# Kernel tuning notes

Measured on AMD Instinct MI355X. Metric: run time of the kernel, lower is better.

Reference implementation:

```python
import jax, jax.numpy as jnp
import numpy as np

NUM_POPS = 8
K_ACTIVE = 2
IN, OUT = 2048, 2048
BATCH = 8192


def setup_inputs() -> dict:
    key = jax.random.key(0)
    ks = jax.random.split(key, 5)
    scale_in = 1.0 / np.sqrt(IN)
    return {
        "x": jax.random.normal(ks[0], (BATCH, IN), dtype=jnp.float32),
        # expert (population) linear params, stacked: W[p] is [OUT, IN]
        "W": jax.random.uniform(ks[1], (NUM_POPS, OUT, IN), dtype=jnp.float32, minval=-scale_in, maxval=scale_in),
        "b": jax.random.uniform(ks[2], (NUM_POPS, OUT), dtype=jnp.float32, minval=-scale_in, maxval=scale_in),
        # selector linear params
        "Ws": jax.random.uniform(ks[3], (NUM_POPS, IN), dtype=jnp.float32, minval=-scale_in, maxval=scale_in),
        "bs": jax.random.uniform(ks[4], (NUM_POPS,), dtype=jnp.float32, minval=-scale_in, maxval=scale_in),
    }


def reference(x, W, b, Ws, bs):
    # Eval-path math of SimplifiedDRNLayer: per-sample top-k expert selection,
    # uniform mean over the k selected experts' linear outputs.
    logits = x @ Ws.T + bs                      # [B, P]
    probs = jax.nn.softmax(logits, axis=-1)     # [B, P]
    _, topk_idx = jax.lax.top_k(probs, K_ACTIVE)  # [B, k] int32
    # combine weights: 1/k on selected experts, 0 elsewhere
    mask = jax.nn.one_hot(topk_idx, NUM_POPS, dtype=x.dtype).sum(axis=1) / K_ACTIVE  # [B, P]
    # all-expert outputs (P is small/fixed); [B, P, OUT]
    ys = jnp.einsum("poi,bi->bpo", W, x) + b
    out = jnp.einsum("bp,bpo->bo", mask, ys)    # [B, OUT]
    return out
```

## Files before the change

### kernel.cpp

```cpp
#include <hip/hip_runtime.h>
#include <stdint.h>

#define B_ROWS 8192
#define K_DIM 2048
#define N_DIM 2048
#define NPOP 8

typedef float f32x4 __attribute__((ext_vector_type(4)));
typedef __bf16 bf16x8 __attribute__((ext_vector_type(8)));

__device__ __forceinline__ unsigned short f2bf(float f) {
  unsigned int u = __float_as_uint(f);
  u += 0x7fffu + ((u >> 16) & 1u);
  return (unsigned short)(u >> 16);
}

__device__ __forceinline__ void glds16(const unsigned short* g, unsigned short* l) {
  __builtin_amdgcn_global_load_lds(
      (__attribute__((address_space(1))) unsigned int*)g,
      (__attribute__((address_space(3))) unsigned int*)l, 16, 0, 0);
}

__global__ void prep_w_kernel(const float* __restrict__ W, unsigned short* __restrict__ Wb) {
  const int n4 = NPOP * N_DIM * K_DIM / 4;
  int stride = gridDim.x * blockDim.x;
  for (int i = blockIdx.x * blockDim.x + threadIdx.x; i < n4; i += stride) {
    float4 v = reinterpret_cast<const float4*>(W)[i];
    ushort4 s;
    s.x = f2bf(v.x); s.y = f2bf(v.y); s.z = f2bf(v.z); s.w = f2bf(v.w);
    reinterpret_cast<ushort4*>(Wb)[i] = s;
  }
}

__global__ void prep_x_sel_kernel(const float* __restrict__ x,
                                  const float* __restrict__ Ws,
                                  const float* __restrict__ bs,
                                  unsigned short* __restrict__ xb,
                                  int* __restrict__ sel,
                                  float* __restrict__ out) {
  {
    float4 z4 = {0.f, 0.f, 0.f, 0.f};
    float4* o4 = reinterpret_cast<float4*>(out);
    const int n4 = B_ROWS * N_DIM / 4;
    int stride = gridDim.x * blockDim.x;
    for (int i = blockIdx.x * blockDim.x + threadIdx.x; i < n4; i += stride) o4[i] = z4;
  }

  const int w = threadIdx.x >> 6;
  const int l = threadIdx.x & 63;
  const int r = blockIdx.x * 4 + w;

  float acc[NPOP];
#pragma unroll
  for (int p = 0; p < NPOP; ++p) acc[p] = 0.f;

  const float4* x4  = reinterpret_cast<const float4*>(x);
  const float4* Ws4 = reinterpret_cast<const float4*>(Ws);
#pragma unroll
  for (int j = 0; j < 8; ++j) {
    int idx = j * 256 + l * 4;
    float4 v = x4[(r * K_DIM + idx) >> 2];
    ushort4 s; s.x = f2bf(v.x); s.y = f2bf(v.y); s.z = f2bf(v.z); s.w = f2bf(v.w);
    *reinterpret_cast<ushort4*>(xb + (size_t)r * K_DIM + idx) = s;
#pragma unroll
    for (int p = 0; p < NPOP; ++p) {
      float4 wv = Ws4[(p * K_DIM + idx) >> 2];
      acc[p] += v.x * wv.x + v.y * wv.y + v.z * wv.z + v.w * wv.w;
    }
  }
#pragma unroll
  for (int off = 32; off > 0; off >>= 1)
#pragma unroll
    for (int p = 0; p < NPOP; ++p) acc[p] += __shfl_xor(acc[p], off, 64);

  if (l == 0) {
    float lg[NPOP];
#pragma unroll
    for (int p = 0; p < NPOP; ++p) lg[p] = acc[p] + bs[p];
    int p1 = 0;
#pragma unroll
    for (int p = 1; p < NPOP; ++p) if (lg[p] > lg[p1]) p1 = p;
    int p2 = -1;
#pragma unroll
    for (int p = 0; p < NPOP; ++p) {
      if (p == p1) continue;
      if (p2 < 0 || lg[p] > lg[p2]) p2 = p;
    }
    sel[r] = p1 * 8 + p2;
  }
}

__global__ __launch_bounds__(256) void build_lists_kernel(const int* __restrict__ sel,
                                                          int* __restrict__ lists,
                                                          int* __restrict__ cnt) {
  const int ex = blockIdx.x;
  const int t  = threadIdx.x;

  __shared__ int psum[256];

  int local[32];
  int c = 0;
#pragma unroll
  for (int i = 0; i < 32; ++i) {
    int r = i * 256 + t;
    int s = sel[r];
    if ((s >> 3) == ex || (s & 7) == ex) local[c++] = r;
  }
  psum[t] = c;
  __syncthreads();
  for (int off = 1; off < 256; off <<= 1) {
    int v = (t >= off) ? psum[t - off] : 0;
    __syncthreads();
    psum[t] += v;
    __syncthreads();
  }
  int start = psum[t] - c;
  for (int i = 0; i < c; ++i) lists[ex * 8192 + start + i] = local[i];
  if (t == 255) cnt[ex] = psum[255];
}


#define BAR()  asm volatile("s_barrier" ::: "memory")
#define VMW8   asm volatile("s_waitcnt vmcnt(8)" ::: "memory")
#define VMW0   asm volatile("s_waitcnt vmcnt(0)" ::: "memory")
#define SP(x)  __builtin_amdgcn_s_setprio(x)
#define SB0()  __builtin_amdgcn_sched_barrier(0)

#define STAGE_A(buf, msel, kt) do {                                            \
    unsigned short* lb_ = &As[buf][(msel) * 2048 + w * 512];                   \
    glds16((const unsigned short*)((const char*)xb + (aoff##msel##0 + (unsigned)((kt) * 128))), lb_); \
    glds16((const unsigned short*)((const char*)xb + (aoff##msel##1 + (unsigned)((kt) * 128))), lb_ + 4096); \
  } while (0)

#define STAGE_B(buf, nsel, kt) do {                                            \
    unsigned short* lb_ = &Bs[buf][(nsel) * 2048 + w * 512];                   \
    glds16((const unsigned short*)(bgp + (boff##nsel##0 + (unsigned)((kt) * 128))), lb_); \
    glds16((const unsigned short*)(bgp + (boff##nsel##1 + (unsigned)((kt) * 128))), lb_ + 4096); \
  } while (0)

#define LOAD_AF(buf, msel) do {                                                \
    const char* ab_ = (const char*)&As[0][0] + (buf) * 16384 + (msel) * 4096 + arow_rd; \
    _Pragma("unroll") for (int mi_ = 0; mi_ < 2; ++mi_) {                      \
      af[mi_][0] = *(const bf16x8*)(ab_ + mi_ * 2048 + csw0);                  \
      af[mi_][1] = *(const bf16x8*)(ab_ + mi_ * 2048 + csw1); }                \
  } while (0)

#define LOAD_BF(dst, buf, nsel) do {                                           \
    const char* bb_ = (const char*)&Bs[0][0] + (buf) * 16384 + (nsel) * 4096 + brow_rd; \
    _Pragma("unroll") for (int ni_ = 0; ni_ < 2; ++ni_) {                      \
      dst[ni_][0] = *(const bf16x8*)(bb_ + ni_ * 2048 + csw0);                 \
      dst[ni_][1] = *(const bf16x8*)(bb_ + ni_ * 2048 + csw1); }               \
  } while (0)

#define MMA(msel, nsel, bfv) do {                                              \
    _Pragma("unroll") for (int mi_ = 0; mi_ < 2; ++mi_)                        \
    _Pragma("unroll") for (int ni_ = 0; ni_ < 2; ++ni_) {                      \
      f32x4 a_ = acc[(msel)*2+mi_][(nsel)*2+ni_];                              \
      a_ = __builtin_amdgcn_mfma_f32_16x16x32_bf16(af[mi_][0], bfv[ni_][0], a_, 0, 0, 0); \
      a_ = __builtin_amdgcn_mfma_f32_16x16x32_bf16(af[mi_][1], bfv[ni_][1], a_, 0, 0, 0); \
      acc[(msel)*2+mi_][(nsel)*2+ni_] = a_; }                                  \
  } while (0)

#define HALF_ITER(buf, kt, DOS, VM) do {                                       \
    LOAD_AF(buf, 0); LOAD_BF(bf0, buf, 0);                                     \
    BAR(); SP(1); MMA(0, 0, bf0); SP(0); SB0(); BAR();                         \
    LOAD_BF(bf1, buf, 1);                                                      \
    if (DOS) { STAGE_A(buf, 0, (kt) + 2); STAGE_B(buf, 0, (kt) + 2); }         \
    BAR(); SP(1); MMA(0, 1, bf1); SP(0); SB0(); BAR();                         \
    LOAD_AF(buf, 1);                                                           \
    if (DOS) STAGE_B(buf, 1, (kt) + 2);                                        \
    BAR(); SP(1); MMA(1, 1, bf1); SP(0); SB0(); BAR();                         \
    if (DOS) STAGE_A(buf, 1, (kt) + 2);                                        \
    VM;                                                                        \
    BAR(); SP(1); MMA(1, 0, bf0); SP(0); SB0(); BAR();                         \
  } while (0)

#define EPILOGUE()                                                             \
  _Pragma("unroll") for (int a = 0; a < 4; ++a) {                              \
    _Pragma("unroll") for (int j = 0; j < 4; ++j) {                            \
      int r = m0 + wm * 64 + a * 16 + (quad << 2) + j;                         \
      if (r < cg) {                                                            \
        int gr = list[r];                                                      \
        float* orow = out + (size_t)gr * N_DIM + n0 + wn * 64;                 \
        _Pragma("unroll") for (int bq = 0; bq < 4; ++bq) {                     \
          int col = bq * 16 + lane16;                                          \
          float v = 0.5f * acc[a][bq][j] + bv[bq];                             \
          (void)unsafeAtomicAdd(&orow[col], v);                                \
        } } } }

__global__ __launch_bounds__(256, 2) void gemm_kernel(
    const unsigned short* __restrict__ xb,
    const unsigned short* __restrict__ Wb,
    const float* __restrict__ bvec,
    const int* __restrict__ lists,
    const int* __restrict__ cnt,
    float* __restrict__ out) {
  const int bid = blockIdx.x;
  const int g   = bid & 7;
  const int mt  = (bid >> 3) & 63;
  const int nt  = bid >> 9;
  const int cg  = cnt[g];
  const int m0  = mt * 128;
  if (m0 >= cg) return;
  const int n0 = nt * 128;

  __shared__ __align__(16) unsigned short As[2][8192];
  __shared__ __align__(16) unsigned short Bs[2][8192];

  const int t = threadIdx.x;
  const int w = t >> 6, l = t & 63;
  const int lane16 = l & 15, quad = l >> 4;
  const int wm = w >> 1, wn = w & 1;
  const int l8 = l >> 3;
  const unsigned int swS = (unsigned)(((l & 7) ^ l8) << 4);
  const unsigned int swR = (unsigned)((l & 7) << 4);
  const unsigned int csw0 = ((unsigned)(quad << 4)) ^ swR;
  const unsigned int csw1 = ((unsigned)(64 | (quad << 4))) ^ swR;
  const unsigned int arow_rd = (unsigned)(wm * 8192 + lane16 * 128);
  const unsigned int brow_rd = (unsigned)(wn * 8192 + lane16 * 128);

  const int* list = lists + g * 8192;
  const char* bgp = (const char*)(Wb + (size_t)g * (N_DIM * K_DIM));

  const int trb = w * 8 + l8;
  int r00 = m0 + trb;       int g00 = (r00 < cg) ? list[r00] : 0;
  int r01 = m0 + 64 + trb;  int g01 = (r01 < cg) ? list[r01] : 0;
  int r10 = m0 + 32 + trb;  int g10 = (r10 < cg) ? list[r10] : 0;
  int r11 = m0 + 96 + trb;  int g11 = (r11 < cg) ? list[r11] : 0;
  const unsigned int aoff00 = (unsigned)g00 * 4096u + swS;
  const unsigned int aoff01 = (unsigned)g01 * 4096u + swS;
  const unsigned int aoff10 = (unsigned)g10 * 4096u + swS;
  const unsigned int aoff11 = (unsigned)g11 * 4096u + swS;
  const unsigned int boff00 = (unsigned)(n0 + trb)      * 4096u + swS;
  const unsigned int boff01 = (unsigned)(n0 + 64 + trb) * 4096u + swS;
  const unsigned int boff10 = (unsigned)(n0 + 32 + trb) * 4096u + swS;
  const unsigned int boff11 = (unsigned)(n0 + 96 + trb) * 4096u + swS;

  bf16x8 af[2][2], bf0[2][2], bf1[2][2];
  f32x4 acc[4][4];
#pragma unroll
  for (int i = 0; i < 4; ++i)
#pragma unroll
    for (int jq = 0; jq < 4; ++jq) { f32x4 z = {0.f, 0.f, 0.f, 0.f}; acc[i][jq] = z; }

  STAGE_A(0, 0, 0); STAGE_B(0, 0, 0); STAGE_B(0, 1, 0); STAGE_A(0, 1, 0);
  STAGE_A(1, 0, 1); STAGE_B(1, 0, 1); STAGE_B(1, 1, 1); STAGE_A(1, 1, 1);
  VMW8;
  BAR();

#pragma unroll 1
  for (int h = 0; h < 30; h += 2) {
    HALF_ITER(0, h,     1, VMW8);
    HALF_ITER(1, h + 1, 1, VMW8);
  }
  HALF_ITER(0, 30, 0, VMW0);
  HALF_ITER(1, 31, 0, (void)0);

  const float* bias = bvec + (size_t)g * N_DIM + n0 + wn * 64;
  float bv[4];
#pragma unroll
  for (int bq = 0; bq < 4; ++bq) bv[bq] = 0.5f * bias[bq * 16 + lane16];

  EPILOGUE();
}

extern "C" void kernel_launch(void* const* d_in, const int* in_sizes, int n_in,
                              void* d_out, int out_size, void* d_ws, size_t ws_size,
                              hipStream_t stream) {
  const float* x  = (const float*)d_in[0];
  const float* W  = (const float*)d_in[1];
  const float* b  = (const float*)d_in[2];
  const float* Ws = (const float*)d_in[3];
  const float* bs = (const float*)d_in[4];
  float* out = (float*)d_out;

  char* ws = (char*)d_ws;
  unsigned short* Wb = (unsigned short*)ws;
  unsigned short* xb = (unsigned short*)(ws + (size_t)67108864);
  int* lists = (int*)(ws + (size_t)67108864 + 33554432);
  int* cnt   = (int*)(ws + (size_t)67108864 + 33554432 + 262144);
  int* sel   = (int*)(ws + (size_t)67108864 + 33554432 + 262144 + 4096);

  prep_w_kernel<<<4096, 256, 0, stream>>>(W, Wb);
  prep_x_sel_kernel<<<2048, 256, 0, stream>>>(x, Ws, bs, xb, sel, out);
  build_lists_kernel<<<8, 256, 0, stream>>>(sel, lists, cnt);
  gemm_kernel<<<dim3(8192), dim3(256), 0, stream>>>(xb, Wb, b, lists, cnt, out);
}
```

Before: 540.7 us.

## Fuse prep kernels and restructure GEMM main loop into two MMA phases

Merges the weight-conversion and x/selector prep kernels into one launch, with blocks beyond 2048 exiting after the grid-stride W conversion and output zeroing. The GEMM half-iteration now does two MMA groups per barrier pair instead of four. The A-half-1 tile for the next k-step is staged one step ahead into the other buffer, and the remaining stages are issued after the second fragment load, with the wait count adjusted to 6. This cuts barrier count and launch overhead, but the shorter prefetch distance for one A tile and larger MMA groups may expose more load latency.

```diff
diff --git a/kernel.cpp b/kernel.cpp
--- a/kernel.cpp
+++ b/kernel.cpp
@@ -21,31 +21,35 @@
       (__attribute__((address_space(3))) unsigned int*)l, 16, 0, 0);
 }
 
-__global__ void prep_w_kernel(const float* __restrict__ W, unsigned short* __restrict__ Wb) {
-  const int n4 = NPOP * N_DIM * K_DIM / 4;
-  int stride = gridDim.x * blockDim.x;
-  for (int i = blockIdx.x * blockDim.x + threadIdx.x; i < n4; i += stride) {
-    float4 v = reinterpret_cast<const float4*>(W)[i];
-    ushort4 s;
-    s.x = f2bf(v.x); s.y = f2bf(v.y); s.z = f2bf(v.z); s.w = f2bf(v.w);
-    reinterpret_cast<ushort4*>(Wb)[i] = s;
-  }
-}
-
-__global__ void prep_x_sel_kernel(const float* __restrict__ x,
-                                  const float* __restrict__ Ws,
-                                  const float* __restrict__ bs,
-                                  unsigned short* __restrict__ xb,
-                                  int* __restrict__ sel,
-                                  float* __restrict__ out) {
+__global__ __launch_bounds__(256) void prep_all_kernel(
+    const float* __restrict__ x,
+    const float* __restrict__ W,
+    const float* __restrict__ Ws,
+    const float* __restrict__ bs,
+    unsigned short* __restrict__ xb,
+    unsigned short* __restrict__ Wb,
+    int* __restrict__ sel,
+    float* __restrict__ out) {
+  const int tid  = blockIdx.x * 256 + threadIdx.x;
+  const int nthr = gridDim.x * 256;
+
+  {
+    const int n4 = NPOP * N_DIM * K_DIM / 4;
+    for (int i = tid; i < n4; i += nthr) {
+      float4 v = reinterpret_cast<const float4*>(W)[i];
+      ushort4 s;
+      s.x = f2bf(v.x); s.y = f2bf(v.y); s.z = f2bf(v.z); s.w = f2bf(v.w);
+      reinterpret_cast<ushort4*>(Wb)[i] = s;
+    }
+  }
   {
     float4 z4 = {0.f, 0.f, 0.f, 0.f};
     float4* o4 = reinterpret_cast<float4*>(out);
     const int n4 = B_ROWS * N_DIM / 4;
-    int stride = gridDim.x * blockDim.x;
-    for (int i = blockIdx.x * blockDim.x + threadIdx.x; i < n4; i += stride) o4[i] = z4;
-  }
-
+    for (int i = tid; i < n4; i += nthr) o4[i] = z4;
+  }
+
+  if (blockIdx.x >= 2048) return;
   const int w = threadIdx.x >> 6;
   const int l = threadIdx.x & 63;
   const int r = blockIdx.x * 4 + w;
@@ -121,7 +125,7 @@
 
 
 #define BAR()  asm volatile("s_barrier" ::: "memory")
-#define VMW8   asm volatile("s_waitcnt vmcnt(8)" ::: "memory")
+#define VMW6   asm volatile("s_waitcnt vmcnt(6)" ::: "memory")
 #define VMW0   asm volatile("s_waitcnt vmcnt(0)" ::: "memory")
 #define SP(x)  __builtin_amdgcn_s_setprio(x)
 #define SB0()  __builtin_amdgcn_sched_barrier(0)
@@ -161,18 +165,15 @@
       acc[(msel)*2+mi_][(nsel)*2+ni_] = a_; }                                  \
   } while (0)
 
-#define HALF_ITER(buf, kt, DOS, VM) do {                                       \
-    LOAD_AF(buf, 0); LOAD_BF(bf0, buf, 0);                                     \
-    BAR(); SP(1); MMA(0, 0, bf0); SP(0); SB0(); BAR();                         \
-    LOAD_BF(bf1, buf, 1);                                                      \
-    if (DOS) { STAGE_A(buf, 0, (kt) + 2); STAGE_B(buf, 0, (kt) + 2); }         \
-    BAR(); SP(1); MMA(0, 1, bf1); SP(0); SB0(); BAR();                         \
+#define HALF_ITER(buf, kt, DOS1, DOS2, VM) do {                                \
+    LOAD_AF(buf, 0); LOAD_BF(bf0, buf, 0); LOAD_BF(bf1, buf, 1);               \
+    if (DOS1) STAGE_A((buf) ^ 1, 1, (kt) + 1);                                 \
+    BAR(); SP(1); MMA(0, 0, bf0); MMA(0, 1, bf1); SP(0); SB0(); BAR();         \
     LOAD_AF(buf, 1);                                                           \
-    if (DOS) STAGE_B(buf, 1, (kt) + 2);                                        \
-    BAR(); SP(1); MMA(1, 1, bf1); SP(0); SB0(); BAR();                         \
-    if (DOS) STAGE_A(buf, 1, (kt) + 2);                                        \
+    if (DOS2) { STAGE_A(buf, 0, (kt) + 2); STAGE_B(buf, 0, (kt) + 2);          \
+                STAGE_B(buf, 1, (kt) + 2); }                                   \
     VM;                                                                        \
-    BAR(); SP(1); MMA(1, 0, bf0); SP(0); SB0(); BAR();                         \
+    BAR(); SP(1); MMA(1, 1, bf1); MMA(1, 0, bf0); SP(0); SB0(); BAR();         \
   } while (0)
 
 #define EPILOGUE()                                                             \
@@ -244,17 +245,17 @@
     for (int jq = 0; jq < 4; ++jq) { f32x4 z = {0.f, 0.f, 0.f, 0.f}; acc[i][jq] = z; }
 
   STAGE_A(0, 0, 0); STAGE_B(0, 0, 0); STAGE_B(0, 1, 0); STAGE_A(0, 1, 0);
-  STAGE_A(1, 0, 1); STAGE_B(1, 0, 1); STAGE_B(1, 1, 1); STAGE_A(1, 1, 1);
-  VMW8;
+  STAGE_A(1, 0, 1); STAGE_B(1, 0, 1); STAGE_B(1, 1, 1);
+  VMW6;
   BAR();
 
 #pragma unroll 1
   for (int h = 0; h < 30; h += 2) {
-    HALF_ITER(0, h,     1, VMW8);
-    HALF_ITER(1, h + 1, 1, VMW8);
-  }
-  HALF_ITER(0, 30, 0, VMW0);
-  HALF_ITER(1, 31, 0, (void)0);
+    HALF_ITER(0, h,     1, 1, VMW6);
+    HALF_ITER(1, h + 1, 1, 1, VMW6);
+  }
+  HALF_ITER(0, 30, 1, 0, VMW0);
+  HALF_ITER(1, 31, 0, 0, (void)0);
 
   const float* bias = bvec + (size_t)g * N_DIM + n0 + wn * 64;
   float bv[4];
@@ -281,8 +282,7 @@
   int* cnt   = (int*)(ws + (size_t)67108864 + 33554432 + 262144);
   int* sel   = (int*)(ws + (size_t)67108864 + 33554432 + 262144 + 4096);
 
-  prep_w_kernel<<<4096, 256, 0, stream>>>(W, Wb);
-  prep_x_sel_kernel<<<2048, 256, 0, stream>>>(x, Ws, bs, xb, sel, out);
+  prep_all_kernel<<<4096, 256, 0, stream>>>(x, W, Ws, bs, xb, Wb, sel, out);
   build_lists_kernel<<<8, 256, 0, stream>>>(sel, lists, cnt);
   gemm_kernel<<<dim3(8192), dim3(256), 0, stream>>>(xb, Wb, b, lists, cnt, out);
 }
```

New measurement: 511.3 us. -5.4%, faster.
